# Optimization experiments

Hardware: AMD Instinct MI355X
Metric: run time of the kernel (lower is better)

## Reference

```python
import jax, jax.numpy as jnp
import numpy as np

N = 50000      # nodes
M = 800000     # edges
D = 128        # node_state_dim == msg_dim
EF = 32        # edge_feat_dim
DF = 32        # node_dist_feat_dim
ATT = 128      # att_hidden_dim
L = 2          # num_layer (num_prop = 1)
IN = D + EF + DF  # 192, MLP input dim


def setup_inputs() -> dict:
    key = jax.random.key(0)
    ks = jax.random.split(key, 18)
    rn = lambda k, shape, s=0.05: jax.random.normal(k, shape, dtype=jnp.float32) * s
    return {
        "node_feat":   rn(ks[0], (N, D), 1.0),
        "node_feat_c": rn(ks[1], (N, D), 1.0),
        "edge":        jax.random.randint(ks[2], (M, 2), 0, N, dtype=jnp.int32),
        "edge_feat":   rn(ks[3], (M, EF), 1.0),
        "dist_feat":   rn(ks[4], (M, DF), 1.0),
        # msg MLP: Linear(IN->D) -> ReLU -> Linear(D->D), stacked over layers
        "msg_w0": rn(ks[5], (L, IN, D)),  "msg_b0": jnp.zeros((L, D), jnp.float32),
        "msg_w1": rn(ks[6], (L, D, D)),   "msg_b1": jnp.zeros((L, D), jnp.float32),
        # attention head: Linear(IN->ATT) -> ReLU -> Linear(ATT->D) -> Sigmoid
        "att_w0": rn(ks[7], (L, IN, ATT)), "att_b0": jnp.zeros((L, ATT), jnp.float32),
        "att_w1": rn(ks[8], (L, ATT, D)),  "att_b1": jnp.zeros((L, D), jnp.float32),
        # LSTMCell params (torch layout: W_ih [4H, in], W_hh [4H, H], gate order i,f,g,o)
        "lstm_wih": rn(ks[9],  (L, 4 * D, D)),
        "lstm_whh": rn(ks[10], (L, 4 * D, D)),
        "lstm_bih": jnp.zeros((L, 4 * D), jnp.float32),
        "lstm_bhh": jnp.zeros((L, 4 * D), jnp.float32),
    }


def _lstm_cell(x, h, c, wih, whh, bih, bhh):
    gates = x @ wih.T + bih + h @ whh.T + bhh          # [N, 4D]
    i, f, g, o = jnp.split(gates, 4, axis=1)
    c2 = jax.nn.sigmoid(f) * c + jax.nn.sigmoid(i) * jnp.tanh(g)
    h2 = jax.nn.sigmoid(o) * jnp.tanh(c2)
    return h2, c2


def reference(node_feat, node_feat_c, edge, edge_feat, dist_feat,
              msg_w0, msg_b0, msg_w1, msg_b1,
              att_w0, att_b0, att_w1, att_b1,
              lstm_wih, lstm_whh, lstm_bih, lstm_bhh):
    src = edge[:, 0]
    dst = edge[:, 1]
    state, state_c = node_feat, node_feat_c
    for ii in range(L):
        if ii > 0:
            state = jax.nn.relu(state)
        # _prop (num_prop = 1)
        state_diff = state[src] - state[dst]                               # [M, D]
        edge_input = jnp.concatenate([state_diff, edge_feat, dist_feat], 1)  # [M, IN]
        msg = jax.nn.relu(edge_input @ msg_w0[ii] + msg_b0[ii]) @ msg_w1[ii] + msg_b1[ii]
        att = jax.nn.sigmoid(
            jax.nn.relu(edge_input @ att_w0[ii] + att_b0[ii]) @ att_w1[ii] + att_b1[ii])
        msg = msg * att
        state_msg = jax.ops.segment_sum(msg, dst, num_segments=N)          # scatter_add
        state, state_c = _lstm_cell(state_msg, state, state_c,
                                    lstm_wih[ii], lstm_whh[ii],
                                    lstm_bih[ii], lstm_bhh[ii])
    return state
```

## Files before the change

### kernel.cpp

```cpp
#include <hip/hip_runtime.h>
#include <hip/hip_bf16.h>

constexpr int N  = 50000;
constexpr int M  = 800000;
constexpr int D  = 128;
constexpr int IN = 192;
constexpr int TE = 128;
constexpr int NCH = 10;
constexpr int NBLK = (N + 255) / 256;

typedef __attribute__((ext_vector_type(4)))  short short4v;
typedef __attribute__((ext_vector_type(8)))  short short8;
typedef __attribute__((ext_vector_type(16))) float f32x16;
typedef _Float16 half8  __attribute__((ext_vector_type(8)));

__device__ __align__(16) short g_wp[163840];
__device__ __align__(16) short g_lw[262144];
__device__ __align__(16) short g_efdf[(size_t)M * 64];
__device__ __align__(16) short g_sbf[(size_t)N * D];
__device__ int g_cnt[N];
__device__ int g_part[NBLK];
__device__ int g_ssrc[M];
__device__ int g_sdst[M];
__device__ int g_inv[M];

__device__ __forceinline__ float sigm(float x) { return 1.0f / (1.0f + __expf(-x)); }

__device__ __forceinline__ short f2bf(float f) {
    unsigned u = __builtin_bit_cast(unsigned, f);
    u = (u + 0x7FFFu + ((u >> 16) & 1u)) >> 16;
    return (short)u;
}
__device__ __forceinline__ unsigned pk2(float a, float b) {
    __hip_bfloat162 h = __float22bfloat162_rn(float2{a, b});
    unsigned u;
    __builtin_memcpy(&u, &h, 4);
    return u;
}
__device__ __forceinline__ unsigned pkh(float a, float b) {
    auto h = __builtin_amdgcn_cvt_pkrtz(a, b);
    unsigned u;
    __builtin_memcpy(&u, &h, 4);
    return u;
}
__device__ __forceinline__ short f2h(float f) {
    _Float16 h = (_Float16)f;
    return __builtin_bit_cast(short, h);
}
__device__ __forceinline__ float h2f(short s) {
    _Float16 h = __builtin_bit_cast(_Float16, s);
    return (float)h;
}

__global__ void zero_cnt_kernel() {
    for (int i = blockIdx.x * 256 + threadIdx.x; i < N; i += gridDim.x * 256) g_cnt[i] = 0;
}
__global__ void hist_kernel(const int* __restrict__ edge) {
    int e = blockIdx.x * 256 + threadIdx.x;
    if (e < M) atomicAdd(&g_cnt[edge[e * 2 + 1]], 1);
}
__global__ void scanA_kernel() {
    __shared__ int red[256];
    const int t = threadIdx.x;
    const int idx = blockIdx.x * 256 + t;
    red[t] = (idx < N) ? g_cnt[idx] : 0;
    __syncthreads();
#pragma unroll
    for (int s = 128; s > 0; s >>= 1) {
        if (t < s) red[t] += red[t + s];
        __syncthreads();
    }
    if (t == 0) g_part[blockIdx.x] = red[0];
}
__global__ void scanB_kernel() {
    __shared__ int sh[256];
    const int t = threadIdx.x;
    int v = (t < NBLK) ? g_part[t] : 0;
    sh[t] = v;
    __syncthreads();
    int x = v;
    for (int s = 1; s < 256; s <<= 1) {
        int y = (t >= s) ? sh[t - s] : 0;
        __syncthreads();
        x += y; sh[t] = x;
        __syncthreads();
    }
    if (t < NBLK) g_part[t] = x - v;
}
__global__ void scanC_kernel() {
    __shared__ int sh[256];
    const int t = threadIdx.x;
    const int idx = blockIdx.x * 256 + t;
    int v = (idx < N) ? g_cnt[idx] : 0;
    sh[t] = v;
    __syncthreads();
    int x = v;
    for (int s = 1; s < 256; s <<= 1) {
        int y = (t >= s) ? sh[t - s] : 0;
        __syncthreads();
        x += y; sh[t] = x;
        __syncthreads();
    }
    if (idx < N) g_cnt[idx] = g_part[blockIdx.x] + x - v;
}
__global__ void scatter_kernel(const int* __restrict__ edge) {
    int e = blockIdx.x * 256 + threadIdx.x;
    if (e < M) {
        const int s = edge[e * 2], d = edge[e * 2 + 1];
        const int p = atomicAdd(&g_cnt[d], 1);
        g_ssrc[p] = s;
        g_sdst[p] = d;
        g_inv[p]  = e;
    }
}

__global__ void pack_edge(const float* __restrict__ w0m, const float* __restrict__ w0a,
                          const float* __restrict__ w1m, const float* __restrict__ w1a) {
    int gid = blockIdx.x * 256 + threadIdx.x;
    int ii = gid / 81920;
    int r  = gid % 81920;
    int p  = r / 40960;  r %= 40960;
    int which = (r >= 24576) ? 1 : 0;
    int r2 = which ? r - 24576 : r;
    int e    = r2 & 7;
    int f    = r2 >> 3;
    int lane = f & 63;
    int ktct = f >> 6;
    int ct = ktct & 3, kt = ktct >> 2;
    int k   = kt * 16 + ((lane >> 5) << 3) + e;
    int col = ct * 32 + (lane & 31);
    const float* w0 = p ? w0a : w0m;
    const float* w1 = p ? w1a : w1m;
    float v = which ? w1[((size_t)ii * D + k) * D + col]
                    : w0[((size_t)ii * IN + k) * D + col];
    g_wp[gid] = f2h(v);
}

__global__ void pack_lstm(const float* __restrict__ wih, const float* __restrict__ whh) {
    int gid = blockIdx.x * 256 + threadIdx.x;
    int ii = gid >> 17;
    int r  = gid & 131071;
    int e = r & 7, f = r >> 3;
    int lane = f & 63, rest = f >> 6;
    int cf = rest & 15, kt = rest >> 4;
    int col = cf * 32 + (lane & 31);
    int k   = (kt & 7) * 16 + ((lane >> 5) << 3) + e;
    const float* src = (kt < 8) ? wih : whh;
    g_lw[gid] = f2bf(src[((size_t)ii * 512 + col) * D + k]);
}

__global__ void pack_efdf(const float* __restrict__ ef, const float* __restrict__ df) {
    int gid = blockIdx.x * 256 + threadIdx.x;
    int p = gid >> 3, c0 = (gid & 7) * 8;
    const int e = g_inv[p];
    const float* s = (c0 < 32) ? (ef + (size_t)e * 32 + c0) : (df + (size_t)e * 32 + (c0 - 32));
    float4 u0 = *(const float4*)s, u1 = *(const float4*)(s + 4);
    short8 t;
    unsigned* tp = (unsigned*)&t;
    tp[0] = pkh(u0.x, u0.y); tp[1] = pkh(u0.z, u0.w);
    tp[2] = pkh(u1.x, u1.y); tp[3] = pkh(u1.z, u1.w);
    *(short8*)(g_efdf + (size_t)gid * 8) = t;
}

__global__ void init_kernel(const float4* __restrict__ nf, const float4* __restrict__ nfc,
                            float4* __restrict__ state, float4* __restrict__ state_c) {
    const int total = N * D / 4;
    for (int i = blockIdx.x * blockDim.x + threadIdx.x; i < total; i += gridDim.x * blockDim.x) {
        state[i]   = nf[i];
        state_c[i] = nfc[i];
    }
}

__global__ void prep_kernel(float4* __restrict__ state, float4* __restrict__ msg, int do_relu) {
    const int total = N * D / 4;
    const float4 z = make_float4(0.f, 0.f, 0.f, 0.f);
    for (int i = blockIdx.x * blockDim.x + threadIdx.x; i < total; i += gridDim.x * blockDim.x) {
        float4 v = state[i];
        if (do_relu) {
            v.x = fmaxf(v.x, 0.f); v.y = fmaxf(v.y, 0.f);
            v.z = fmaxf(v.z, 0.f); v.w = fmaxf(v.w, 0.f);
            state[i] = v;
        }
        short4v b;
        unsigned* bp = (unsigned*)&b;
        bp[0] = pkh(v.x, v.y); bp[1] = pkh(v.z, v.w);
        *(short4v*)(g_sbf + (size_t)i * 4) = b;
        msg[i] = z;
    }
}

#define MFMA16(a, b, c) __builtin_amdgcn_mfma_f32_32x32x16_f16(a, b, c, 0, 0, 0)
#define MFMABF(a, b, c) __builtin_amdgcn_mfma_f32_32x32x16_bf16(a, b, c, 0, 0, 0)

template<int BASE, int NC>
__device__ __forceinline__ void gemmA(const short8* __restrict__ gsrc, short8* wb,
                                      const half8 a1[12], int tid, int lane, int cg,
                                      f32x16& o0, f32x16& o1) {
    f32x16 acc0 = {}, acc1 = {};
#pragma unroll
    for (int c = 0; c < NC; ++c) {
        const int gc = BASE + c;
        short8 g0, g1;
        if (gc + 1 < NCH) {
            g0 = gsrc[(size_t)(gc + 1) * 1024 + tid];
            g1 = gsrc[(size_t)(gc + 1) * 1024 + tid + 512];
        }
        const short8* buf = wb + (gc & 1) * 1024;
#pragma unroll
        for (int kl = 0; kl < 4; ++kl) {
            half8 b0 = __builtin_bit_cast(half8, buf[(kl * 4 + cg * 2 + 0) * 64 + lane]);
            half8 b1 = __builtin_bit_cast(half8, buf[(kl * 4 + cg * 2 + 1) * 64 + lane]);
            acc0 = MFMA16(a1[c * 4 + kl], b0, acc0);
            acc1 = MFMA16(a1[c * 4 + kl], b1, acc1);
        }
        if (gc + 1 < NCH) {
            short8* d = wb + ((gc + 1) & 1) * 1024;
            d[tid] = g0; d[tid + 512] = g1;
        }
        __syncthreads();
    }
    o0 = acc0; o1 = acc1;
}

template<int BASE, int NC>
__device__ __forceinline__ void gemmH(const short8* __restrict__ gsrc, short8* wb,
                                      const short (*hsr)[136], int tid, int lane, int cg, int half,
                                      f32x16& o0, f32x16& o1) {
    f32x16 acc0 = {}, acc1 = {};
#pragma unroll
    for (int c = 0; c < NC; ++c) {
        const int gc = BASE + c;
        short8 g0, g1;
        if (gc + 1 < NCH) {
            g0 = gsrc[(size_t)(gc + 1) * 1024 + tid];
            g1 = gsrc[(size_t)(gc + 1) * 1024 + tid + 512];
        }
        const short8* buf = wb + (gc & 1) * 1024;
#pragma unroll
        for (int kl = 0; kl < 4; ++kl) {
            const int kt = c * 4 + kl;
            half8 a2 = __builtin_bit_cast(half8, *(const short8*)&hsr[lane & 31][kt * 16 + half]);
            half8 b0 = __builtin_bit_cast(half8, buf[(kl * 4 + cg * 2 + 0) * 64 + lane]);
            half8 b1 = __builtin_bit_cast(half8, buf[(kl * 4 + cg * 2 + 1) * 64 + lane]);
            acc0 = MFMA16(a2, b0, acc0);
            acc1 = MFMA16(a2, b1, acc1);
        }
        if (gc + 1 < NCH) {
            short8* d = wb + ((gc + 1) & 1) * 1024;
            d[tid] = g0; d[tid + 512] = g1;
        }
        __syncthreads();
    }
    o0 = acc0; o1 = acc1;
}

__device__ __forceinline__ void hwrite(short (*hsr)[136], const f32x16& a0, const f32x16& a1v,
                                       const float* __restrict__ b0, int lane, int cg) {
#pragma unroll
    for (int ct = 0; ct < 2; ++ct) {
        const int col = cg * 64 + ct * 32 + (lane & 31);
        const float bv = b0[col];
        f32x16 a = ct ? a1v : a0;
#pragma unroll
        for (int rp = 0; rp < 8; ++rp) {
            const int reg = rp * 2;
            const int row = (reg & 3) + 8 * (reg >> 2) + 4 * (lane >> 5);
            const unsigned pr = pkh(fmaxf(a[reg] + bv, 0.f), fmaxf(a[reg + 1] + bv, 0.f));
            hsr[row][col]     = (short)(pr & 0xFFFF);
            hsr[row + 1][col] = (short)(pr >> 16);
        }
    }
}

__global__ __launch_bounds__(512, 4)
void edge_mfma(int ii,
               const float* __restrict__ b0m, const float* __restrict__ b1m,
               const float* __restrict__ b0a, const float* __restrict__ b1a,
               float* __restrict__ state_msg) {
    __shared__ __align__(16) char pool[68096];
    short8* wb = (short8*)pool;
    short (*hs)[32][136] = (short(*)[32][136])(pool + 32768);
    int* sdst = (int*)(pool + 67584);

    const int tid  = threadIdx.x;
    const int lane = tid & 63;
    const int w    = tid >> 6;
    const int rt   = w >> 1;
    const int cg   = w & 1;
    const int e0   = blockIdx.x * TE;

    if (tid < TE) sdst[tid] = g_sdst[e0 + tid];

    const int er   = e0 + rt * 32 + (lane & 31);
    const int half = (lane >> 5) << 3;
    const int s  = g_ssrc[er];
    const int d2 = g_sdst[er];
    const short* srow = g_sbf + (size_t)s  * D;
    const short* drow = g_sbf + (size_t)d2 * D;
    half8 a1[12];
#pragma unroll
    for (int kt = 0; kt < 8; ++kt) {
        const int k0 = kt * 16 + half;
        half8 sv = __builtin_bit_cast(half8, *(const short8*)(srow + k0));
        half8 dv = __builtin_bit_cast(half8, *(const short8*)(drow + k0));
        a1[kt] = sv - dv;
    }
#pragma unroll
    for (int kt = 8; kt < 12; ++kt)
        a1[kt] = __builtin_bit_cast(half8, *(const short8*)(g_efdf + (size_t)er * 64 + (kt - 8) * 16 + half));

    const short8* gsrc = (const short8*)(g_wp + (size_t)ii * 81920);

    wb[tid] = gsrc[tid];
    wb[tid + 512] = gsrc[tid + 512];
    __syncthreads();

    f32x16 t0, t1, m0, m1, c0, c1;
    gemmA<0, 3>(gsrc, wb, a1, tid, lane, cg, t0, t1);
    hwrite(hs[rt], t0, t1, b0m, lane, cg);
    __syncthreads();
    gemmH<3, 2>(gsrc, wb, hs[rt], tid, lane, cg, half, m0, m1);

    unsigned mb[16];
#pragma unroll
    for (int ct = 0; ct < 2; ++ct) {
        const float bm = b1m[cg * 64 + ct * 32 + (lane & 31)];
        f32x16 mv = ct ? m1 : m0;
#pragma unroll
        for (int rp = 0; rp < 8; ++rp)
            mb[ct * 8 + rp] = pkh(mv[rp * 2] + bm, mv[rp * 2 + 1] + bm);
    }

    gemmA<5, 3>(gsrc, wb, a1, tid, lane, cg, t0, t1);
    hwrite(hs[rt], t0, t1, b0a, lane, cg);
    __syncthreads();
    gemmH<8, 2>(gsrc, wb, hs[rt], tid, lane, cg, half, c0, c1);

    float (*vt)[132] = (float(*)[132])pool;
    const int colr = tid & 127;
    const int sub  = tid >> 7;
#pragma unroll
    for (int pass = 0; pass < 2; ++pass) {
        if ((rt >> 1) == pass) {
#pragma unroll
            for (int ct = 0; ct < 2; ++ct) {
                const int col = cg * 64 + ct * 32 + (lane & 31);
                const float ba = b1a[col];
                f32x16 av = ct ? c1 : c0;
#pragma unroll
                for (int rp = 0; rp < 8; ++rp) {
                    const int reg = rp * 2;
                    const unsigned u = mb[ct * 8 + rp];
                    const int row = (rt & 1) * 32 + (reg & 3) + 8 * (reg >> 2) + 4 * (lane >> 5);
                    vt[row][col]     = h2f((short)(u & 0xFFFF)) * sigm(av[reg] + ba);
                    vt[row + 1][col] = h2f((short)(u >> 16))    * sigm(av[reg + 1] + ba);
                }
            }
        }
        __syncthreads();
        const int gbase = pass * 64 + sub * 16;
        float run = 0.f;
        int cur = sdst[gbase];
#pragma unroll 4
        for (int r = 0; r < 16; ++r) {
            const int dd = sdst[gbase + r];
            if (dd != cur) {
                atomicAdd(state_msg + (size_t)cur * D + colr, run);
                run = 0.f; cur = dd;
            }
            run += vt[sub * 16 + r][colr];
        }
        atomicAdd(state_msg + (size_t)cur * D + colr, run);
        __syncthreads();
    }
}

__global__ __launch_bounds__(256, 4)
void lstm_mfma(const float* __restrict__ x, float* __restrict__ hbuf, float* __restrict__ cbuf,
               int ii,
               const float* __restrict__ bih, const float* __restrict__ bhh) {
    __shared__ short8 wb[2048];
    const int tid  = threadIdx.x;
    const int lane = tid & 63;
    const int w    = tid >> 6;
    const int n0   = blockIdx.x * 32;
    const int half = (lane >> 5) << 3;
    const int nl   = lane & 31;
    const int nld  = min(n0 + nl, N - 1);

    const short8* gsrc = (const short8*)(g_lw + (size_t)ii * 131072);

    {
        short8 g[4];
#pragma unroll
        for (int i = 0; i < 4; ++i) g[i] = gsrc[tid + i * 256];
#pragma unroll
        for (int i = 0; i < 4; ++i) wb[tid + i * 256] = g[i];
        __syncthreads();
    }

    f32x16 acc[4] = {};
#pragma unroll
    for (int kt = 0; kt < 16; ++kt) {
        const float* srow = (kt < 8) ? (x + (size_t)nld * D + kt * 16 + half)
                                     : (hbuf + (size_t)nld * D + (kt - 8) * 16 + half);
        float4 u0 = *(const float4*)(srow);
        float4 u1 = *(const float4*)(srow + 4);
        short8 a;
        unsigned* ap = (unsigned*)&a;
        ap[0] = pk2(u0.x, u0.y); ap[1] = pk2(u0.z, u0.w);
        ap[2] = pk2(u1.x, u1.y); ap[3] = pk2(u1.z, u1.w);

        short8 g[4];
        if (kt + 1 < 16) {
            const short8* p = gsrc + (size_t)(kt + 1) * 1024;
#pragma unroll
            for (int i = 0; i < 4; ++i) g[i] = p[tid + i * 256];
        }
        const short8* buf = wb + (kt & 1) * 1024;
#pragma unroll
        for (int q = 0; q < 4; ++q) {
            short8 b = buf[(q * 4 + w) * 64 + lane];
            acc[q] = MFMABF(a, b, acc[q]);
        }
        if (kt + 1 < 16) {
            short8* d = wb + ((kt + 1) & 1) * 1024;
#pragma unroll
            for (int i = 0; i < 4; ++i) d[tid + i * 256] = g[i];
        }
        __syncthreads();
    }

    const int col = (w << 5) + nl;
    const float bi = bih[col]       + bhh[col];
    const float bf = bih[128 + col] + bhh[128 + col];
    const float bg = bih[256 + col] + bhh[256 + col];
    const float bo = bih[384 + col] + bhh[384 + col];
#pragma unroll
    for (int reg = 0; reg < 16; ++reg) {
        const int nn = (reg & 3) + 8 * (reg >> 2) + 4 * (lane >> 5);
        const int n = n0 + nn;
        if (n < N) {
            const float gi = acc[0][reg] + bi;
            const float gf = acc[1][reg] + bf;
            const float gg = acc[2][reg] + bg;
            const float go = acc[3][reg] + bo;
            float* cp = cbuf + (size_t)n * D + col;
            const float c2 = sigm(gf) * (*cp) + sigm(gi) * tanhf(gg);
            const float h2 = sigm(go) * tanhf(c2);
            *cp = c2;
            hbuf[(size_t)n * D + col] = h2;
        }
    }
}

extern "C" void kernel_launch(void* const* d_in, const int* in_sizes, int n_in,
                              void* d_out, int out_size, void* d_ws, size_t ws_size,
                              hipStream_t stream) {
    const float* node_feat   = (const float*)d_in[0];
    const float* node_feat_c = (const float*)d_in[1];
    const int*   edge        = (const int*)d_in[2];
    const float* edge_feat   = (const float*)d_in[3];
    const float* dist_feat   = (const float*)d_in[4];
    const float* msg_w0 = (const float*)d_in[5];
    const float* msg_b0 = (const float*)d_in[6];
    const float* msg_w1 = (const float*)d_in[7];
    const float* msg_b1 = (const float*)d_in[8];
    const float* att_w0 = (const float*)d_in[9];
    const float* att_b0 = (const float*)d_in[10];
    const float* att_w1 = (const float*)d_in[11];
    const float* att_b1 = (const float*)d_in[12];
    const float* lstm_wih = (const float*)d_in[13];
    const float* lstm_whh = (const float*)d_in[14];
    const float* lstm_bih = (const float*)d_in[15];
    const float* lstm_bhh = (const float*)d_in[16];

    float* state     = (float*)d_out;
    float* state_c   = (float*)d_ws;
    float* state_msg = (float*)d_ws + (size_t)N * D;

    zero_cnt_kernel<<<256, 256, 0, stream>>>();
    hist_kernel<<<(M + 255) / 256, 256, 0, stream>>>(edge);
    scanA_kernel<<<NBLK, 256, 0, stream>>>();
    scanB_kernel<<<1, 256, 0, stream>>>();
    scanC_kernel<<<NBLK, 256, 0, stream>>>();
    scatter_kernel<<<(M + 255) / 256, 256, 0, stream>>>(edge);

    pack_efdf<<<25000, 256, 0, stream>>>(edge_feat, dist_feat);
    pack_edge<<<640, 256, 0, stream>>>(msg_w0, att_w0, msg_w1, att_w1);
    pack_lstm<<<1024, 256, 0, stream>>>(lstm_wih, lstm_whh);

    init_kernel<<<2048, 256, 0, stream>>>((const float4*)node_feat, (const float4*)node_feat_c,
                                          (float4*)state, (float4*)state_c);

    for (int ii = 0; ii < 2; ++ii) {
        prep_kernel<<<2048, 256, 0, stream>>>((float4*)state, (float4*)state_msg, ii > 0 ? 1 : 0);

        edge_mfma<<<M / TE, 512, 0, stream>>>(
            ii,
            msg_b0 + (size_t)ii * D, msg_b1 + (size_t)ii * D,
            att_b0 + (size_t)ii * D, att_b1 + (size_t)ii * D,
            state_msg);

        lstm_mfma<<<(N + 31) / 32, 256, 0, stream>>>(
            state_msg, state, state_c, ii,
            lstm_bih + (size_t)ii * 4 * D, lstm_bhh + (size_t)ii * 4 * D);
    }
}
```

Baseline: 887.8 us.

## Fuse prep into init/LSTM epilogue and deepen weight prefetch to two chunks

Removes the per-layer prep kernel. Init now writes the fp16 state copy and zeroes the message buffer, and the LSTM epilogue applies ReLU, writes the fp16 state and re-zeroes its slice of the message buffer for the next layer. This saves two full passes over node state. The edge GEMM helpers are merged into one templated phase that prefetches weights two chunks ahead in registers instead of one, hiding more global-load latency at the cost of extra registers. One risk is the in-place zeroing of x inside the LSTM kernel after it has been read by the same block.

```diff
diff --git a/kernel.cpp b/kernel.cpp
--- a/kernel.cpp
+++ b/kernel.cpp
@@ -163,24 +163,14 @@
 }
 
 __global__ void init_kernel(const float4* __restrict__ nf, const float4* __restrict__ nfc,
-                            float4* __restrict__ state, float4* __restrict__ state_c) {
-    const int total = N * D / 4;
-    for (int i = blockIdx.x * blockDim.x + threadIdx.x; i < total; i += gridDim.x * blockDim.x) {
-        state[i]   = nf[i];
-        state_c[i] = nfc[i];
-    }
-}
-
-__global__ void prep_kernel(float4* __restrict__ state, float4* __restrict__ msg, int do_relu) {
+                            float4* __restrict__ state, float4* __restrict__ state_c,
+                            float4* __restrict__ msg) {
     const int total = N * D / 4;
     const float4 z = make_float4(0.f, 0.f, 0.f, 0.f);
     for (int i = blockIdx.x * blockDim.x + threadIdx.x; i < total; i += gridDim.x * blockDim.x) {
-        float4 v = state[i];
-        if (do_relu) {
-            v.x = fmaxf(v.x, 0.f); v.y = fmaxf(v.y, 0.f);
-            v.z = fmaxf(v.z, 0.f); v.w = fmaxf(v.w, 0.f);
-            state[i] = v;
-        }
+        float4 v = nf[i];
+        state[i]   = v;
+        state_c[i] = nfc[i];
         short4v b;
         unsigned* bp = (unsigned*)&b;
         bp[0] = pkh(v.x, v.y); bp[1] = pkh(v.z, v.w);
@@ -192,64 +182,39 @@
 #define MFMA16(a, b, c) __builtin_amdgcn_mfma_f32_32x32x16_f16(a, b, c, 0, 0, 0)
 #define MFMABF(a, b, c) __builtin_amdgcn_mfma_f32_32x32x16_bf16(a, b, c, 0, 0, 0)
 
-template<int BASE, int NC>
-__device__ __forceinline__ void gemmA(const short8* __restrict__ gsrc, short8* wb,
-                                      const half8 a1[12], int tid, int lane, int cg,
-                                      f32x16& o0, f32x16& o1) {
+template<int BASE, int NC, bool FROM_H>
+__device__ __forceinline__ void gemm_phase(const short8* __restrict__ gsrc, short8* wb,
+                                           short8 gA[2], const half8 a1[12],
+                                           const short (*hsr)[136],
+                                           int tid, int lane, int cg, int half,
+                                           f32x16& o0, f32x16& o1) {
     f32x16 acc0 = {}, acc1 = {};
 #pragma unroll
     for (int c = 0; c < NC; ++c) {
         const int gc = BASE + c;
-        short8 g0, g1;
-        if (gc + 1 < NCH) {
-            g0 = gsrc[(size_t)(gc + 1) * 1024 + tid];
-            g1 = gsrc[(size_t)(gc + 1) * 1024 + tid + 512];
+        short8 gB0, gB1;
+        if (gc + 2 < NCH) {
+            gB0 = gsrc[(size_t)(gc + 2) * 1024 + tid];
+            gB1 = gsrc[(size_t)(gc + 2) * 1024 + tid + 512];
         }
         const short8* buf = wb + (gc & 1) * 1024;
 #pragma unroll
         for (int kl = 0; kl < 4; ++kl) {
+            const int kt = c * 4 + kl;
+            half8 a = FROM_H
+                ? __builtin_bit_cast(half8, *(const short8*)&hsr[lane & 31][kt * 16 + half])
+                : a1[kt];
             half8 b0 = __builtin_bit_cast(half8, buf[(kl * 4 + cg * 2 + 0) * 64 + lane]);
             half8 b1 = __builtin_bit_cast(half8, buf[(kl * 4 + cg * 2 + 1) * 64 + lane]);
-            acc0 = MFMA16(a1[c * 4 + kl], b0, acc0);
-            acc1 = MFMA16(a1[c * 4 + kl], b1, acc1);
+            acc0 = MFMA16(a, b0, acc0);
+            acc1 = MFMA16(a, b1, acc1);
         }
         if (gc + 1 < NCH) {
             short8* d = wb + ((gc + 1) & 1) * 1024;
-            d[tid] = g0; d[tid + 512] = g1;
-        }
-        __syncthreads();
-    }
-    o0 = acc0; o1 = acc1;
-}
-
-template<int BASE, int NC>
-__device__ __forceinline__ void gemmH(const short8* __restrict__ gsrc, short8* wb,
-                                      const short (*hsr)[136], int tid, int lane, int cg, int half,
-                                      f32x16& o0, f32x16& o1) {
-    f32x16 acc0 = {}, acc1 = {};
-#pragma unroll
-    for (int c = 0; c < NC; ++c) {
-        const int gc = BASE + c;
-        short8 g0, g1;
-        if (gc + 1 < NCH) {
-            g0 = gsrc[(size_t)(gc + 1) * 1024 + tid];
-            g1 = gsrc[(size_t)(gc + 1) * 1024 + tid + 512];
-        }
-        const short8* buf = wb + (gc & 1) * 1024;
-#pragma unroll
-        for (int kl = 0; kl < 4; ++kl) {
-            const int kt = c * 4 + kl;
-            half8 a2 = __builtin_bit_cast(half8, *(const short8*)&hsr[lane & 31][kt * 16 + half]);
-            half8 b0 = __builtin_bit_cast(half8, buf[(kl * 4 + cg * 2 + 0) * 64 + lane]);
-            half8 b1 = __builtin_bit_cast(half8, buf[(kl * 4 + cg * 2 + 1) * 64 + lane]);
-            acc0 = MFMA16(a2, b0, acc0);
-            acc1 = MFMA16(a2, b1, acc1);
-        }
-        if (gc + 1 < NCH) {
-            short8* d = wb + ((gc + 1) & 1) * 1024;
-            d[tid] = g0; d[tid + 512] = g1;
-        }
-        __syncthreads();
+            d[tid] = gA[0]; d[tid + 512] = gA[1];
+        }
+        __syncthreads();
+        if (gc + 2 < NCH) { gA[0] = gB0; gA[1] = gB1; }
     }
     o0 = acc0; o1 = acc1;
 }
@@ -313,13 +278,16 @@
 
     wb[tid] = gsrc[tid];
     wb[tid + 512] = gsrc[tid + 512];
+    short8 gA[2];
+    gA[0] = gsrc[1024 + tid];
+    gA[1] = gsrc[1024 + tid + 512];
     __syncthreads();
 
     f32x16 t0, t1, m0, m1, c0, c1;
-    gemmA<0, 3>(gsrc, wb, a1, tid, lane, cg, t0, t1);
+    gemm_phase<0, 3, false>(gsrc, wb, gA, a1, hs[rt], tid, lane, cg, half, t0, t1);
     hwrite(hs[rt], t0, t1, b0m, lane, cg);
     __syncthreads();
-    gemmH<3, 2>(gsrc, wb, hs[rt], tid, lane, cg, half, m0, m1);
+    gemm_phase<3, 2, true>(gsrc, wb, gA, a1, hs[rt], tid, lane, cg, half, m0, m1);
 
     unsigned mb[16];
 #pragma unroll
@@ -331,10 +299,10 @@
             mb[ct * 8 + rp] = pkh(mv[rp * 2] + bm, mv[rp * 2 + 1] + bm);
     }
 
-    gemmA<5, 3>(gsrc, wb, a1, tid, lane, cg, t0, t1);
+    gemm_phase<5, 3, false>(gsrc, wb, gA, a1, hs[rt], tid, lane, cg, half, t0, t1);
     hwrite(hs[rt], t0, t1, b0a, lane, cg);
     __syncthreads();
-    gemmH<8, 2>(gsrc, wb, hs[rt], tid, lane, cg, half, c0, c1);
+    gemm_phase<8, 2, true>(gsrc, wb, gA, a1, hs[rt], tid, lane, cg, half, c0, c1);
 
     float (*vt)[132] = (float(*)[132])pool;
     const int colr = tid & 127;
@@ -376,8 +344,8 @@
 }
 
 __global__ __launch_bounds__(256, 4)
-void lstm_mfma(const float* __restrict__ x, float* __restrict__ hbuf, float* __restrict__ cbuf,
-               int ii,
+void lstm_mfma(float* __restrict__ x, float* __restrict__ hbuf, float* __restrict__ cbuf,
+               int ii, int last,
                const float* __restrict__ bih, const float* __restrict__ bhh) {
     __shared__ short8 wb[2048];
     const int tid  = threadIdx.x;
@@ -449,7 +417,19 @@
             const float c2 = sigm(gf) * (*cp) + sigm(gi) * tanhf(gg);
             const float h2 = sigm(go) * tanhf(c2);
             *cp = c2;
-            hbuf[(size_t)n * D + col] = h2;
+            const float ho = last ? h2 : fmaxf(h2, 0.f);
+            hbuf[(size_t)n * D + col] = ho;
+            if (!last) g_sbf[(size_t)n * D + col] = f2h(ho);
+        }
+    }
+
+    if (!last) {
+        float4* xr = (float4*)(x + (size_t)n0 * D);
+        const float4 z = make_float4(0.f, 0.f, 0.f, 0.f);
+#pragma unroll
+        for (int i = 0; i < 4; ++i) {
+            const int idx = tid + i * 256;
+            if (n0 + (idx >> 5) < N) xr[idx] = z;
         }
     }
 }
@@ -491,11 +471,9 @@
     pack_lstm<<<1024, 256, 0, stream>>>(lstm_wih, lstm_whh);
 
     init_kernel<<<2048, 256, 0, stream>>>((const float4*)node_feat, (const float4*)node_feat_c,
-                                          (float4*)state, (float4*)state_c);
+                                          (float4*)state, (float4*)state_c, (float4*)state_msg);
 
     for (int ii = 0; ii < 2; ++ii) {
-        prep_kernel<<<2048, 256, 0, stream>>>((float4*)state, (float4*)state_msg, ii > 0 ? 1 : 0);
-
         edge_mfma<<<M / TE, 512, 0, stream>>>(
             ii,
             msg_b0 + (size_t)ii * D, msg_b1 + (size_t)ii * D,
@@ -503,7 +481,7 @@
             state_msg);
 
         lstm_mfma<<<(N + 31) / 32, 256, 0, stream>>>(
-            state_msg, state, state_c, ii,
+            state_msg, state, state_c, ii, (ii == 1) ? 1 : 0,
             lstm_bih + (size_t)ii * 4 * D, lstm_bhh + (size_t)ii * 4 * D);
     }
 }
```

New measurement: 858.2 us. 3.3% less time.
